# Performance work log

Hardware: AMD Instinct MI355X
Metric: run time of the kernel (lower is better)

Reference implementation:

```python
import jax, jax.numpy as jnp
import numpy as np

N_EMBD = 512
N_HEADS = 8
D_HEAD = N_EMBD // N_HEADS


def setup_inputs() -> dict:
    key = jax.random.key(0)
    k1, k2, k3, k4, k5 = jax.random.split(key, 5)
    B, T = 4, 2048
    scale = 1.0 / np.sqrt(N_EMBD)
    return {
        "x": jax.random.normal(k1, (B, T, N_EMBD), dtype=jnp.float32),
        # fused QKV projection: Linear(n_embd, 3*n_embd)
        "W_attn": jax.random.normal(k2, (N_EMBD, 3 * N_EMBD), dtype=jnp.float32) * scale,
        "b_attn": jax.random.normal(k3, (3 * N_EMBD,), dtype=jnp.float32) * 0.01,
        # output projection: Linear(n_embd, n_embd)
        "W_out": jax.random.normal(k4, (N_EMBD, N_EMBD), dtype=jnp.float32) * scale,
        "b_out": jax.random.normal(k5, (N_EMBD,), dtype=jnp.float32) * 0.01,
    }


def reference(x, W_attn, b_attn, W_out, b_out):
    B, T, C = x.shape
    # fused QKV projection then split
    qkv = x @ W_attn + b_attn  # [B, T, 3C]
    q, k, v = jnp.split(qkv, 3, axis=-1)
    # [B, T, C] -> [B, H, T, Dh]
    def heads(t):
        return t.reshape(B, T, N_HEADS, D_HEAD).transpose(0, 2, 1, 3)
    q, k, v = heads(q), heads(k), heads(v)
    # scaled dot-product attention (non-causal, no mask; dropout off in eval)
    scores = jnp.einsum("bhqd,bhkd->bhqk", q, k) / jnp.sqrt(jnp.float32(D_HEAD))
    attn = jax.nn.softmax(scores, axis=-1)
    y = jnp.einsum("bhqk,bhkd->bhqd", attn, v)  # [B, H, T, Dh]
    y = y.transpose(0, 2, 1, 3).reshape(B, T, C)
    # output projection (resid dropout off in eval)
    return y @ W_out + b_out
```

## Files before the change

kernel.cpp:

```cpp
#include <hip/hip_runtime.h>

typedef __attribute__((ext_vector_type(8))) short bf16x8;
typedef __attribute__((ext_vector_type(4))) float f32x4;
typedef unsigned short u16;
typedef unsigned int u32;

#define MFMA16(A, B, C) __builtin_amdgcn_mfma_f32_16x16x32_bf16((A), (B), (C), 0, 0, 0)

#if __has_builtin(__builtin_amdgcn_exp2f)
#define EXP2(x) __builtin_amdgcn_exp2f(x)
#else
#define EXP2(x) exp2f(x)
#endif

typedef __attribute__((address_space(3))) unsigned int lds_u32;
typedef const __attribute__((address_space(1))) unsigned int glb_u32;

__device__ __forceinline__ u16 f2bf(float f) {
  union { float f; unsigned u; } x; x.f = f;
  unsigned r = (x.u + 0x7fffu + ((x.u >> 16) & 1u)) >> 16;
  return (u16)r;
}
__device__ __forceinline__ float bf2f(u16 h) {
  union { float f; unsigned u; } x; x.u = ((unsigned)h) << 16;
  return x.f;
}

__device__ __forceinline__ void stage_sw64(const u16* src, u16* lds, int tid) {
#pragma unroll
  for (int i = 0; i < 2; i++) {
    int vv = tid + i * 256;
    int row = vv >> 3, c = vv & 7;
    const u16* gp = src + (size_t)row * 64 + (size_t)(c ^ (row & 7)) * 8;
    __builtin_amdgcn_global_load_lds((glb_u32*)gp,
        (lds_u32*)(lds + (size_t)(i * 256 + (tid & 192)) * 8), 16, 0, 0);
  }
}

__device__ __forceinline__ void stage_lin64(const u16* src, u16* lds, int tid) {
#pragma unroll
  for (int i = 0; i < 2; i++) {
    const u16* gp = src + (size_t)(i * 256 + tid) * 8;
    __builtin_amdgcn_global_load_lds((glb_u32*)gp,
        (lds_u32*)(lds + (size_t)(i * 256 + (tid & 192)) * 8), 16, 0, 0);
  }
}

template <int ROWS>
__device__ __forceinline__ void stage_ld512(const u16* src, u16* lds, int tid) {
#pragma unroll
  for (int i = 0; i < ROWS / 32; i++) {
    int vv = tid + i * 256;
    int row = vv >> 3, c = vv & 7;
    const u16* gp = src + (size_t)row * 512 + (size_t)(c ^ (row & 7)) * 8;
    __builtin_amdgcn_global_load_lds((glb_u32*)gp,
        (lds_u32*)(lds + (size_t)(i * 256 + (tid & 192)) * 8), 16, 0, 0);
  }
}

__global__ __launch_bounds__(256) void prep_kernel(const float* __restrict__ x,
                                                   u16* __restrict__ xb,
                                                   const float* __restrict__ Wa,
                                                   u16* __restrict__ wta,
                                                   const float* __restrict__ Wo,
                                                   u16* __restrict__ whi,
                                                   u16* __restrict__ wlo) {
  __shared__ u16 Th[64][72];
  __shared__ u16 Tl[64][72];
  const int bid = blockIdx.x;
  const int tid = threadIdx.x;

  if (bid < 4096) {
    int i = bid * 256 + tid;
    float4 v = ((const float4*)x)[i];
    ushort4 o;
    o.x = f2bf(v.x); o.y = f2bf(v.y); o.z = f2bf(v.z); o.w = f2bf(v.w);
    ((ushort4*)xb)[i] = o;
    return;
  }

  if (bid < 4288) {
    const int t = bid - 4096;
    const int n0 = (t % 24) * 64;
    const int k0 = (t / 24) * 64;
    const int r = tid >> 4, c4 = (tid & 15) * 4;
#pragma unroll
    for (int i = 0; i < 4; i++) {
      int row = r + i * 16;
      float4 v = *(const float4*)&Wa[(size_t)(k0 + row) * 1536 + n0 + c4];
      Th[c4 + 0][row] = f2bf(v.x);
      Th[c4 + 1][row] = f2bf(v.y);
      Th[c4 + 2][row] = f2bf(v.z);
      Th[c4 + 3][row] = f2bf(v.w);
    }
    __syncthreads();
    const int row = tid >> 2, c16 = (tid & 3) * 16;
    *(uint4*)&wta[(size_t)(n0 + row) * 512 + k0 + c16]     = *(uint4*)&Th[row][c16];
    *(uint4*)&wta[(size_t)(n0 + row) * 512 + k0 + c16 + 8] = *(uint4*)&Th[row][c16 + 8];
    return;
  }

  {
    const int t = bid - 4288;
    const int n0 = (t & 7) * 64;
    const int k0 = (t >> 3) * 64;
    const int r = tid >> 4, c4 = (tid & 15) * 4;
#pragma unroll
    for (int i = 0; i < 4; i++) {
      int row = r + i * 16;
      float4 v = *(const float4*)&Wo[(size_t)(k0 + row) * 512 + n0 + c4];
      float vv[4] = {v.x, v.y, v.z, v.w};
#pragma unroll
      for (int jj = 0; jj < 4; jj++) {
        u16 hi = f2bf(vv[jj]);
        Th[c4 + jj][row] = hi;
        Tl[c4 + jj][row] = f2bf(vv[jj] - bf2f(hi));
      }
    }
    __syncthreads();
    const int row = tid >> 2, c16 = (tid & 3) * 16;
    *(uint4*)&whi[(size_t)(n0 + row) * 512 + k0 + c16]     = *(uint4*)&Th[row][c16];
    *(uint4*)&whi[(size_t)(n0 + row) * 512 + k0 + c16 + 8] = *(uint4*)&Th[row][c16 + 8];
    *(uint4*)&wlo[(size_t)(n0 + row) * 512 + k0 + c16]     = *(uint4*)&Tl[row][c16];
    *(uint4*)&wlo[(size_t)(n0 + row) * 512 + k0 + c16 + 8] = *(uint4*)&Tl[row][c16 + 8];
  }
}

__global__ __launch_bounds__(256) void gemm_qkv(const u16* __restrict__ xb,
                                                const u16* __restrict__ wta,
                                                const float* __restrict__ b_attn,
                                                u16* __restrict__ q,
                                                u16* __restrict__ kk,
                                                u16* __restrict__ v) {
  __shared__ u16 Smem[18432];
  const int bid = blockIdx.x;
  const int xcd = bid & 7, rr = bid >> 3;
  const int m0 = (xcd * 8 + (rr & 7)) * 128;
  const int n0 = (rr >> 3) * 128;
  const int tid  = threadIdx.x;
  const int lane = tid & 63, w = tid >> 6;
  const int wm = w >> 1, wn = w & 1;
  const int quad = lane >> 4, l15 = lane & 15;
  const int sw0 = ((quad)     ^ (l15 & 7)) * 8;
  const int sw1 = ((quad + 4) ^ (l15 & 7)) * 8;

  f32x4 acc[4][4] = {};

  for (int kt = 0; kt < 8; kt++) {
    stage_ld512<128>(xb  + (size_t)m0 * 512 + kt * 64, Smem, tid);
    stage_ld512<128>(wta + (size_t)n0 * 512 + kt * 64, Smem + 8192, tid);
    __syncthreads();
#pragma unroll
    for (int ks = 0; ks < 2; ks++) {
      const int sw = ks ? sw1 : sw0;
      bf16x8 af[4], bf[4];
#pragma unroll
      for (int ri = 0; ri < 4; ri++)
        af[ri] = *(const bf16x8*)&Smem[(wm * 64 + ri * 16 + l15) * 64 + sw];
#pragma unroll
      for (int ci = 0; ci < 4; ci++)
        bf[ci] = *(const bf16x8*)&Smem[8192 + (wn * 64 + ci * 16 + l15) * 64 + sw];
#pragma unroll
      for (int ri = 0; ri < 4; ri++)
#pragma unroll
        for (int ci = 0; ci < 4; ci++)
          acc[ri][ci] = MFMA16(af[ri], bf[ci], acc[ri][ci]);
    }
    __syncthreads();
  }

  const float QS = 0.18033688011112043f;
  const int wave_n0 = n0 + wn * 64;
  const int chunk = wave_n0 >> 9;
  const int h = (wave_n0 & 511) >> 6;
  const int m_wave = m0 + wm * 64;
  const int b = m_wave >> 11, t0 = m_wave & 2047;
  const int bh = b * 8 + h;

  if (chunk < 2) {
    u16* T = Smem + w * 4608;
    u16* dst = (chunk == 0) ? q : kk;
    const float scale = (chunk == 0) ? QS : 1.0f;
#pragma unroll
    for (int ri = 0; ri < 4; ri++)
#pragma unroll
      for (int ci = 0; ci < 4; ci++) {
        float bias = b_attn[wave_n0 + ci * 16 + l15];
#pragma unroll
        for (int r = 0; r < 4; r++) {
          int tl = ri * 16 + quad * 4 + r;
          T[tl * 72 + ci * 16 + l15] = f2bf((acc[ri][ci][r] + bias) * scale);
        }
      }
    u16* gdst = dst + (size_t)(bh * 2048 + t0 + lane) * 64;
#pragma unroll
    for (int j = 0; j < 8; j++)
      *(uint4*)&gdst[j * 8] = *(const uint4*)&T[lane * 72 + j * 8];
  } else {
#pragma unroll
    for (int ri = 0; ri < 4; ri++)
#pragma unroll
      for (int ci = 0; ci < 4; ci++) {
        int n = wave_n0 + ci * 16 + l15;
        float bias = b_attn[n];
        int d = n & 63;
        int tv = t0 + ri * 16 + quad * 4;
        int it = tv >> 7, ks2 = (tv >> 5) & 3, qd = (tv >> 3) & 3, jj = tv & 7;
        ushort4 pk;
        pk.x = f2bf(acc[ri][ci][0] + bias);
        pk.y = f2bf(acc[ri][ci][1] + bias);
        pk.z = f2bf(acc[ri][ci][2] + bias);
        pk.w = f2bf(acc[ri][ci][3] + bias);
        size_t idx = ((((size_t)bh * 16 + it) * 4 + ks2) * 64 + d) * 32 + qd * 8 + jj;
        *(ushort4*)&v[idx] = pk;
      }
  }
}

__global__ __launch_bounds__(256, 4) void flash_attn(const u16* __restrict__ q,
                                                     const u16* __restrict__ k,
                                                     const u16* __restrict__ vt,
                                                     u16* __restrict__ yb) {
  __shared__ u16 Kb[2][64 * 64];
  __shared__ u16 Vb[2][64 * 64];
  __shared__ u16 P_lds[4 * 16 * 64];

  const int flat = blockIdx.y * 16 + blockIdx.x;
  const int bh = (flat & 7) * 4 + ((flat >> 3) & 3);
  const int qt = flat >> 5;

  const int tid  = threadIdx.x;
  const int lane = tid & 63, w = tid >> 6;
  const int quad = lane >> 4, l15 = lane & 15;
  const int sw0 = ((quad)     ^ (l15 & 7)) * 8;
  const int sw1 = ((quad + 4) ^ (l15 & 7)) * 8;

  const u16* qp = q  + (size_t)bh * 131072;
  const u16* kp = k  + (size_t)bh * 131072;
  const u16* vp = vt + (size_t)bh * 131072;

  bf16x8 qf[2];
#pragma unroll
  for (int ks = 0; ks < 2; ks++)
    qf[ks] = *(const bf16x8*)(qp + (size_t)(qt * 64 + w * 16 + l15) * 64 + ks * 32 + quad * 8);

  f32x4 l_acc = {};
  f32x4 o[4] = {};

  bf16x8 ones;
  {
    short one = (short)0x3F80;
    ones = (bf16x8){one, one, one, one, one, one, one, one};
  }

  u16* Pw = &P_lds[w * 1024];
  const int psw = l15 & 7;

  stage_sw64(kp, Kb[0], tid);
  stage_lin64(vp, Vb[0], tid);

  for (int it = 0; it < 32; it++) {
    __syncthreads();
    if (it < 31) {
      stage_sw64(kp + (size_t)(it + 1) * 4096, Kb[(it + 1) & 1], tid);
      stage_lin64(vp + (size_t)(it + 1) * 4096, Vb[(it + 1) & 1], tid);
    }
    const u16* Kc = Kb[it & 1];
    const u16* Vc = Vb[it & 1];

#pragma unroll
    for (int jt = 0; jt < 4; jt++) {
      bf16x8 kf0 = *(const bf16x8*)&Kc[(jt * 16 + l15) * 64 + sw0];
      bf16x8 kf1 = *(const bf16x8*)&Kc[(jt * 16 + l15) * 64 + sw1];
      f32x4 s = {0.f, 0.f, 0.f, 0.f};
      s = MFMA16(kf0, qf[0], s);
      s = MFMA16(kf1, qf[1], s);
      u32 pb[4];
#pragma unroll
      for (int r = 0; r < 4; r++) pb[r] = __float_as_uint(EXP2(s[r]));
      uint2 pk;
      pk.x = __builtin_amdgcn_perm(pb[1], pb[0], 0x07060302u);
      pk.y = __builtin_amdgcn_perm(pb[3], pb[2], 0x07060302u);
      int c = jt * 2 + (quad >> 1);
      *(uint2*)&Pw[l15 * 64 + ((c ^ psw) << 3) + (quad & 1) * 4] = pk;
    }

    __builtin_amdgcn_s_setprio(1);
#pragma unroll
    for (int ks = 0; ks < 2; ks++) {
      bf16x8 pf = *(const bf16x8*)&Pw[l15 * 64 + (((ks * 4 + quad) ^ psw) << 3)];
      l_acc = MFMA16(pf, ones, l_acc);
#pragma unroll
      for (int dt = 0; dt < 4; dt++) {
        bf16x8 vf = *(const bf16x8*)&Vc[ks * 2048 + (dt * 16 + l15) * 32 + quad * 8];
        o[dt] = MFMA16(pf, vf, o[dt]);
      }
    }
    __builtin_amdgcn_s_setprio(0);
  }

  __syncthreads();

  const int b = bh >> 3, h = bh & 7;
  u32* Tw = (u32*)(&Kb[0][0]) + (size_t)w * 1088;
#pragma unroll
  for (int r = 0; r < 4; r++) {
    float inv = 1.f / l_acc[r];
#pragma unroll
    for (int dt = 0; dt < 4; dt++) {
      float val = o[dt][r] * inv;
      u16 hi = f2bf(val);
      u16 lo = f2bf(val - bf2f(hi));
      Tw[(quad * 4 + r) * 68 + dt * 16 + l15] = (u32)hi | ((u32)lo << 16);
    }
  }
  {
    int t = qt * 64 + w * 16 + l15;
    size_t rowb = (size_t)(b * 2048 + t) * 512 + h * 64 + quad * 16;
    uint4 g0 = *(uint4*)&Tw[l15 * 68 + quad * 16 + 0];
    uint4 g1 = *(uint4*)&Tw[l15 * 68 + quad * 16 + 4];
    uint4 g2 = *(uint4*)&Tw[l15 * 68 + quad * 16 + 8];
    uint4 g3 = *(uint4*)&Tw[l15 * 68 + quad * 16 + 12];
    uint4 hi4, lo4;
    hi4.x = __builtin_amdgcn_perm(g0.y, g0.x, 0x05040100u);
    hi4.y = __builtin_amdgcn_perm(g0.w, g0.z, 0x05040100u);
    hi4.z = __builtin_amdgcn_perm(g1.y, g1.x, 0x05040100u);
    hi4.w = __builtin_amdgcn_perm(g1.w, g1.z, 0x05040100u);
    lo4.x = __builtin_amdgcn_perm(g0.y, g0.x, 0x07060302u);
    lo4.y = __builtin_amdgcn_perm(g0.w, g0.z, 0x07060302u);
    lo4.z = __builtin_amdgcn_perm(g1.y, g1.x, 0x07060302u);
    lo4.w = __builtin_amdgcn_perm(g1.w, g1.z, 0x07060302u);
    *(uint4*)&yb[rowb] = hi4;
    *(uint4*)&yb[(size_t)4 * 2048 * 512 + rowb] = lo4;
    hi4.x = __builtin_amdgcn_perm(g2.y, g2.x, 0x05040100u);
    hi4.y = __builtin_amdgcn_perm(g2.w, g2.z, 0x05040100u);
    hi4.z = __builtin_amdgcn_perm(g3.y, g3.x, 0x05040100u);
    hi4.w = __builtin_amdgcn_perm(g3.w, g3.z, 0x05040100u);
    lo4.x = __builtin_amdgcn_perm(g2.y, g2.x, 0x07060302u);
    lo4.y = __builtin_amdgcn_perm(g2.w, g2.z, 0x07060302u);
    lo4.z = __builtin_amdgcn_perm(g3.y, g3.x, 0x07060302u);
    lo4.w = __builtin_amdgcn_perm(g3.w, g3.z, 0x07060302u);
    *(uint4*)&yb[rowb + 8] = hi4;
    *(uint4*)&yb[(size_t)4 * 2048 * 512 + rowb + 8] = lo4;
  }
}

__global__ __launch_bounds__(256) void gemm_out(const u16* __restrict__ yhi,
                                                const u16* __restrict__ ylo,
                                                const u16* __restrict__ whi,
                                                const u16* __restrict__ wlo,
                                                const float* __restrict__ b_out,
                                                float* __restrict__ out) {
  __shared__ u16 Ah[128 * 64];
  __shared__ u16 Al[128 * 64];
  __shared__ u16 Bh[64 * 64];
  __shared__ u16 Bl[64 * 64];
  const int bid = blockIdx.x;
  const int xcd = bid & 7, rr = bid >> 3;
  const int m0 = (xcd * 8 + (rr & 7)) * 128;
  const int n0 = (rr >> 3) * 64;
  const int tid  = threadIdx.x;
  const int lane = tid & 63, w = tid >> 6;
  const int wm = w >> 1, wn = w & 1;
  const int quad = lane >> 4, l15 = lane & 15;
  const int sw0 = ((quad)     ^ (l15 & 7)) * 8;
  const int sw1 = ((quad + 4) ^ (l15 & 7)) * 8;

  f32x4 acc[4][2] = {};

  for (int kt = 0; kt < 8; kt++) {
    const int k0 = kt * 64;
    stage_ld512<128>(yhi + (size_t)m0 * 512 + k0, Ah, tid);
    stage_ld512<128>(ylo + (size_t)m0 * 512 + k0, Al, tid);
    stage_ld512<64>(whi + (size_t)n0 * 512 + k0, Bh, tid);
    stage_ld512<64>(wlo + (size_t)n0 * 512 + k0, Bl, tid);
    __syncthreads();
#pragma unroll
    for (int ks = 0; ks < 2; ks++) {
      const int sw = ks ? sw1 : sw0;
      bf16x8 afh[4], afl[4], bfh[2], bfl[2];
#pragma unroll
      for (int ri = 0; ri < 4; ri++) {
        afh[ri] = *(const bf16x8*)&Ah[(wm * 64 + ri * 16 + l15) * 64 + sw];
        afl[ri] = *(const bf16x8*)&Al[(wm * 64 + ri * 16 + l15) * 64 + sw];
      }
#pragma unroll
      for (int ci = 0; ci < 2; ci++) {
        bfh[ci] = *(const bf16x8*)&Bh[(wn * 32 + ci * 16 + l15) * 64 + sw];
        bfl[ci] = *(const bf16x8*)&Bl[(wn * 32 + ci * 16 + l15) * 64 + sw];
      }
#pragma unroll
      for (int ri = 0; ri < 4; ri++)
#pragma unroll
        for (int ci = 0; ci < 2; ci++) {
          acc[ri][ci] = MFMA16(afh[ri], bfh[ci], acc[ri][ci]);
          acc[ri][ci] = MFMA16(afh[ri], bfl[ci], acc[ri][ci]);
          acc[ri][ci] = MFMA16(afl[ri], bfh[ci], acc[ri][ci]);
        }
    }
    __syncthreads();
  }

#pragma unroll
  for (int ri = 0; ri < 4; ri++) {
#pragma unroll
    for (int ci = 0; ci < 2; ci++) {
      int n = n0 + wn * 32 + ci * 16 + l15;
      float bias = b_out[n];
#pragma unroll
      for (int r = 0; r < 4; r++) {
        int m = m0 + wm * 64 + ri * 16 + quad * 4 + r;
        out[(size_t)m * 512 + n] = acc[ri][ci][r] + bias;
      }
    }
  }
}

extern "C" void kernel_launch(void* const* d_in, const int* in_sizes, int n_in,
                              void* d_out, int out_size, void* d_ws, size_t ws_size,
                              hipStream_t stream) {
  const float* x      = (const float*)d_in[0];
  const float* W_attn = (const float*)d_in[1];
  const float* b_attn = (const float*)d_in[2];
  const float* W_out  = (const float*)d_in[3];
  const float* b_out  = (const float*)d_in[4];
  float* out = (float*)d_out;

  char* ws = (char*)d_ws;
  u16* xb   = (u16*)(ws + 0);
  u16* wta  = (u16*)(ws + 8388608);
  u16* wtoh = (u16*)(ws + 9961472);
  u16* wtol = (u16*)(ws + 10485760);
  u16* qb   = (u16*)(ws + 11010048);
  u16* kb   = (u16*)(ws + 19398656);
  u16* vtb  = (u16*)(ws + 27787264);
  u16* yhi  = (u16*)(ws + 36175872);

  prep_kernel<<<4352, 256, 0, stream>>>(x, xb, W_attn, wta, W_out, wtoh, wtol);
  gemm_qkv<<<768, 256, 0, stream>>>(xb, wta, b_attn, qb, kb, vtb);
  flash_attn<<<dim3(16, 64), 256, 0, stream>>>(qb, kb, vtb, yhi);
  gemm_out<<<512, 256, 0, stream>>>(yhi, yhi + (size_t)4 * 2048 * 512, wtoh, wtol, b_out, out);
}
```

Baseline: 175.5 us.

## Process two 16-row query tiles per wave in flash attention with 128-thread blocks

Flash attention now launches 128 threads (2 waves) per block, and each wave handles 32 query rows instead of 16. Each K and V fragment read from LDS is reused for two query sub-tiles, halving LDS fragment reads per MFMA. Staging of K/V tiles is spread over fewer threads, with more loads each. The trade-offs are higher register pressure (two sets of accumulators), fewer waves per block to hide latency, and a launch bound lowered to 2 blocks per CU.

```diff
diff --git a/kernel.cpp b/kernel.cpp
--- a/kernel.cpp
+++ b/kernel.cpp
@@ -37,15 +37,6 @@
   }
 }
 
-__device__ __forceinline__ void stage_lin64(const u16* src, u16* lds, int tid) {
-#pragma unroll
-  for (int i = 0; i < 2; i++) {
-    const u16* gp = src + (size_t)(i * 256 + tid) * 8;
-    __builtin_amdgcn_global_load_lds((glb_u32*)gp,
-        (lds_u32*)(lds + (size_t)(i * 256 + (tid & 192)) * 8), 16, 0, 0);
-  }
-}
-
 template <int ROWS>
 __device__ __forceinline__ void stage_ld512(const u16* src, u16* lds, int tid) {
 #pragma unroll
@@ -55,6 +46,25 @@
     const u16* gp = src + (size_t)row * 512 + (size_t)(c ^ (row & 7)) * 8;
     __builtin_amdgcn_global_load_lds((glb_u32*)gp,
         (lds_u32*)(lds + (size_t)(i * 256 + (tid & 192)) * 8), 16, 0, 0);
+  }
+}
+
+__device__ __forceinline__ void stage_sw64_128(const u16* src, u16* lds, int tid) {
+#pragma unroll
+  for (int i = 0; i < 4; i++) {
+    int vv = tid + i * 128;
+    int row = vv >> 3, c = vv & 7;
+    const u16* gp = src + (size_t)row * 64 + (size_t)(c ^ (row & 7)) * 8;
+    __builtin_amdgcn_global_load_lds((glb_u32*)gp,
+        (lds_u32*)(lds + (size_t)(i * 128 + (tid & 64)) * 8), 16, 0, 0);
+  }
+}
+__device__ __forceinline__ void stage_lin64_128(const u16* src, u16* lds, int tid) {
+#pragma unroll
+  for (int i = 0; i < 4; i++) {
+    const u16* gp = src + (size_t)(i * 128 + tid) * 8;
+    __builtin_amdgcn_global_load_lds((glb_u32*)gp,
+        (lds_u32*)(lds + (size_t)(i * 128 + (tid & 64)) * 8), 16, 0, 0);
   }
 }
 
@@ -217,13 +227,13 @@
   }
 }
 
-__global__ __launch_bounds__(256, 4) void flash_attn(const u16* __restrict__ q,
+__global__ __launch_bounds__(128, 2) void flash_attn(const u16* __restrict__ q,
                                                      const u16* __restrict__ k,
                                                      const u16* __restrict__ vt,
                                                      u16* __restrict__ yb) {
   __shared__ u16 Kb[2][64 * 64];
   __shared__ u16 Vb[2][64 * 64];
-  __shared__ u16 P_lds[4 * 16 * 64];
+  __shared__ u16 P_lds[2 * 2 * 1024];
 
   const int flat = blockIdx.y * 16 + blockIdx.x;
   const int bh = (flat & 7) * 4 + ((flat >> 3) & 3);
@@ -239,13 +249,15 @@
   const u16* kp = k  + (size_t)bh * 131072;
   const u16* vp = vt + (size_t)bh * 131072;
 
-  bf16x8 qf[2];
-#pragma unroll
-  for (int ks = 0; ks < 2; ks++)
-    qf[ks] = *(const bf16x8*)(qp + (size_t)(qt * 64 + w * 16 + l15) * 64 + ks * 32 + quad * 8);
-
-  f32x4 l_acc = {};
-  f32x4 o[4] = {};
+  bf16x8 qf[2][2];
+#pragma unroll
+  for (int qh = 0; qh < 2; qh++)
+#pragma unroll
+    for (int ks = 0; ks < 2; ks++)
+      qf[qh][ks] = *(const bf16x8*)(qp + (size_t)(qt * 64 + w * 32 + qh * 16 + l15) * 64 + ks * 32 + quad * 8);
+
+  f32x4 l_acc[2] = {};
+  f32x4 o[2][4] = {};
 
   bf16x8 ones;
   {
@@ -253,17 +265,17 @@
     ones = (bf16x8){one, one, one, one, one, one, one, one};
   }
 
-  u16* Pw = &P_lds[w * 1024];
+  u16* Pw = &P_lds[w * 2048];
   const int psw = l15 & 7;
 
-  stage_sw64(kp, Kb[0], tid);
-  stage_lin64(vp, Vb[0], tid);
+  stage_sw64_128(kp, Kb[0], tid);
+  stage_lin64_128(vp, Vb[0], tid);
 
   for (int it = 0; it < 32; it++) {
     __syncthreads();
     if (it < 31) {
-      stage_sw64(kp + (size_t)(it + 1) * 4096, Kb[(it + 1) & 1], tid);
-      stage_lin64(vp + (size_t)(it + 1) * 4096, Vb[(it + 1) & 1], tid);
+      stage_sw64_128(kp + (size_t)(it + 1) * 4096, Kb[(it + 1) & 1], tid);
+      stage_lin64_128(vp + (size_t)(it + 1) * 4096, Vb[(it + 1) & 1], tid);
     }
     const u16* Kc = Kb[it & 1];
     const u16* Vc = Vb[it & 1];
@@ -272,28 +284,34 @@
     for (int jt = 0; jt < 4; jt++) {
       bf16x8 kf0 = *(const bf16x8*)&Kc[(jt * 16 + l15) * 64 + sw0];
       bf16x8 kf1 = *(const bf16x8*)&Kc[(jt * 16 + l15) * 64 + sw1];
-      f32x4 s = {0.f, 0.f, 0.f, 0.f};
-      s = MFMA16(kf0, qf[0], s);
-      s = MFMA16(kf1, qf[1], s);
-      u32 pb[4];
-#pragma unroll
-      for (int r = 0; r < 4; r++) pb[r] = __float_as_uint(EXP2(s[r]));
-      uint2 pk;
-      pk.x = __builtin_amdgcn_perm(pb[1], pb[0], 0x07060302u);
-      pk.y = __builtin_amdgcn_perm(pb[3], pb[2], 0x07060302u);
-      int c = jt * 2 + (quad >> 1);
-      *(uint2*)&Pw[l15 * 64 + ((c ^ psw) << 3) + (quad & 1) * 4] = pk;
+      const int c = jt * 2 + (quad >> 1);
+#pragma unroll
+      for (int qh = 0; qh < 2; qh++) {
+        f32x4 s = {0.f, 0.f, 0.f, 0.f};
+        s = MFMA16(kf0, qf[qh][0], s);
+        s = MFMA16(kf1, qf[qh][1], s);
+        u32 pb[4];
+#pragma unroll
+        for (int r = 0; r < 4; r++) pb[r] = __float_as_uint(EXP2(s[r]));
+        uint2 pk;
+        pk.x = __builtin_amdgcn_perm(pb[1], pb[0], 0x07060302u);
+        pk.y = __builtin_amdgcn_perm(pb[3], pb[2], 0x07060302u);
+        *(uint2*)&Pw[qh * 1024 + l15 * 64 + ((c ^ psw) << 3) + (quad & 1) * 4] = pk;
+      }
     }
 
     __builtin_amdgcn_s_setprio(1);
 #pragma unroll
     for (int ks = 0; ks < 2; ks++) {
-      bf16x8 pf = *(const bf16x8*)&Pw[l15 * 64 + (((ks * 4 + quad) ^ psw) << 3)];
-      l_acc = MFMA16(pf, ones, l_acc);
+      bf16x8 pf0 = *(const bf16x8*)&Pw[       l15 * 64 + (((ks * 4 + quad) ^ psw) << 3)];
+      bf16x8 pf1 = *(const bf16x8*)&Pw[1024 + l15 * 64 + (((ks * 4 + quad) ^ psw) << 3)];
+      l_acc[0] = MFMA16(pf0, ones, l_acc[0]);
+      l_acc[1] = MFMA16(pf1, ones, l_acc[1]);
 #pragma unroll
       for (int dt = 0; dt < 4; dt++) {
         bf16x8 vf = *(const bf16x8*)&Vc[ks * 2048 + (dt * 16 + l15) * 32 + quad * 8];
-        o[dt] = MFMA16(pf, vf, o[dt]);
+        o[0][dt] = MFMA16(pf0, vf, o[0][dt]);
+        o[1][dt] = MFMA16(pf1, vf, o[1][dt]);
       }
     }
     __builtin_amdgcn_s_setprio(0);
@@ -304,18 +322,19 @@
   const int b = bh >> 3, h = bh & 7;
   u32* Tw = (u32*)(&Kb[0][0]) + (size_t)w * 1088;
 #pragma unroll
-  for (int r = 0; r < 4; r++) {
-    float inv = 1.f / l_acc[r];
-#pragma unroll
-    for (int dt = 0; dt < 4; dt++) {
-      float val = o[dt][r] * inv;
-      u16 hi = f2bf(val);
-      u16 lo = f2bf(val - bf2f(hi));
-      Tw[(quad * 4 + r) * 68 + dt * 16 + l15] = (u32)hi | ((u32)lo << 16);
-    }
-  }
-  {
-    int t = qt * 64 + w * 16 + l15;
+  for (int qh = 0; qh < 2; qh++) {
+#pragma unroll
+    for (int r = 0; r < 4; r++) {
+      float inv = 1.f / l_acc[qh][r];
+#pragma unroll
+      for (int dt = 0; dt < 4; dt++) {
+        float val = o[qh][dt][r] * inv;
+        u16 hi = f2bf(val);
+        u16 lo = f2bf(val - bf2f(hi));
+        Tw[(quad * 4 + r) * 68 + dt * 16 + l15] = (u32)hi | ((u32)lo << 16);
+      }
+    }
+    int t = qt * 64 + w * 32 + qh * 16 + l15;
     size_t rowb = (size_t)(b * 2048 + t) * 512 + h * 64 + quad * 16;
     uint4 g0 = *(uint4*)&Tw[l15 * 68 + quad * 16 + 0];
     uint4 g1 = *(uint4*)&Tw[l15 * 68 + quad * 16 + 4];
@@ -438,6 +457,6 @@
 
   prep_kernel<<<4352, 256, 0, stream>>>(x, xb, W_attn, wta, W_out, wtoh, wtol);
   gemm_qkv<<<768, 256, 0, stream>>>(xb, wta, b_attn, qb, kb, vtb);
-  flash_attn<<<dim3(16, 64), 256, 0, stream>>>(qb, kb, vtb, yhi);
+  flash_attn<<<dim3(16, 64), 128, 0, stream>>>(qb, kb, vtb, yhi);
   gemm_out<<<512, 256, 0, stream>>>(yhi, yhi + (size_t)4 * 2048 * 512, wtoh, wtol, b_out, out);
 }
```

Result: no change. 175.0 us (-0.2%).
